# Optimization experiments

Hardware: AMD Instinct MI355X
Metric: run time of the kernel (lower is better)

## Reference

```python
import jax, jax.numpy as jnp
import numpy as np

IMG_C = 256
GC = 32  # graph_channel; must equal graph feature dim 32 for the residual


def setup_inputs() -> dict:
    key = jax.random.key(0)
    ks = jax.random.split(key, 10)
    B, N, WH_SIDE = 8, 4096, 64
    s = lambda fan_in: 1.0 / np.sqrt(fan_in)
    return {
        "input_graph": jax.random.normal(ks[0], (B, N, GC), jnp.float32),
        "input_image": jax.random.normal(ks[1], (B, IMG_C, WH_SIDE, WH_SIDE), jnp.float32),
        # Conv1d(kernel=1) weights stored as [out, in]
        "Wq": jax.random.uniform(ks[2], (GC, 32), jnp.float32, -s(32), s(32)),
        "bq": jax.random.uniform(ks[3], (GC,), jnp.float32, -s(32), s(32)),
        "Wk": jax.random.uniform(ks[4], (GC, IMG_C), jnp.float32, -s(IMG_C), s(IMG_C)),
        "bk": jax.random.uniform(ks[5], (GC,), jnp.float32, -s(IMG_C), s(IMG_C)),
        "Wv": jax.random.uniform(ks[6], (GC, IMG_C), jnp.float32, -s(IMG_C), s(IMG_C)),
        "bv": jax.random.uniform(ks[7], (GC,), jnp.float32, -s(IMG_C), s(IMG_C)),
        "Wc": jax.random.uniform(ks[8], (GC, GC), jnp.float32, -s(GC), s(GC)),
        "bc": jax.random.uniform(ks[9], (GC,), jnp.float32, -s(GC), s(GC)),
    }


def reference(input_graph, input_image, Wq, bq, Wk, bk, Wv, bv, Wc, bc):
    B, C, W, H = input_image.shape
    img = input_image.reshape(B, C, W * H)                      # [B, C, L]
    # 1x1 conv projections == channel matmuls
    K = jnp.einsum('oc,bcl->bol', Wk, img) + bk[None, :, None]  # [B, GC, L]
    V = jnp.einsum('oc,bcl->bol', Wv, img) + bv[None, :, None]  # [B, GC, L]
    # Q: graph [B, N, 32] -> conv over channel dim -> [B, N, GC]
    Q = jnp.einsum('oc,bnc->bno', Wq, input_graph) + bq[None, None, :]
    att = jnp.einsum('bno,bol->bnl', Q, K) / jnp.sqrt(jnp.float32(GC))  # [B, N, L]
    # NOTE: original softmax is over dim=1 (the node/query axis)
    att = jax.nn.softmax(att, axis=1)
    message = jnp.einsum('bol,bnl->bon', V, att)                # [B, GC, N]
    out = input_graph.transpose(0, 2, 1) + (
        jnp.einsum('oc,bcn->bon', Wc, message) + bc[None, :, None]
    )                                                           # [B, GC, N]
    return out.transpose(0, 2, 1)                               # [B, N, GC]
```

## Files before the change

kernel.cpp:

```cpp
#include <hip/hip_runtime.h>

#define BB 8
#define NN 4096
#define LL 4096
#define CC 256

typedef short bf16x8 __attribute__((ext_vector_type(8)));
typedef _Float16 f16x8 __attribute__((ext_vector_type(8)));
typedef __fp16 hf16x2 __attribute__((ext_vector_type(2)));
typedef float f32x4 __attribute__((ext_vector_type(4)));

__device__ __forceinline__ short f2bf(float f) {
  union { float f; unsigned u; } v; v.f = f;
  unsigned r = v.u + 0x7fffu + ((v.u >> 16) & 1u);
  return (short)(r >> 16);
}
__device__ __forceinline__ bf16x8 ld8(const float* __restrict__ fp) {
  float4 a = *(const float4*)fp;
  float4 b = *(const float4*)(fp + 4);
  bf16x8 r;
  r[0] = f2bf(a.x); r[1] = f2bf(a.y); r[2] = f2bf(a.z); r[3] = f2bf(a.w);
  r[4] = f2bf(b.x); r[5] = f2bf(b.y); r[6] = f2bf(b.z); r[7] = f2bf(b.w);
  return r;
}

__global__ __launch_bounds__(256) void ka_proj(
    const float* __restrict__ graph, const float* __restrict__ img,
    const float* __restrict__ Wq, const float* __restrict__ bq,
    const float* __restrict__ Wk, const float* __restrict__ bk,
    const float* __restrict__ Wv, const float* __restrict__ bv,
    short* __restrict__ Qb, short* __restrict__ Kt, _Float16* __restrict__ Vt,
    float* __restrict__ Zbuf)
{
  const int tid = threadIdx.x;
  const int w = tid >> 6, lane = tid & 63, lo = lane & 15, q = lane >> 4;
  const int bid = blockIdx.x;
  if (bid < 512) {
    const int b = bid >> 6;
    if (tid < 64) Zbuf[(size_t)b * LL + ((bid & 63) << 6) + tid] = 0.0f;
    const int lt = ((bid & 63) << 6) + (w << 4);
    f32x4 aK0 = {0,0,0,0}, aK1 = {0,0,0,0}, aV0 = {0,0,0,0}, aV1 = {0,0,0,0};
    const float* ib = img + (size_t)b * CC * LL + lt + lo;
    #pragma unroll
    for (int cs = 0; cs < 8; ++cs) {
      const int c0 = cs * 32 + q * 8;
      bf16x8 bi;
      #pragma unroll
      for (int j = 0; j < 8; ++j) bi[j] = f2bf(ib[(size_t)(c0 + j) * LL]);
      bf16x8 wk0 = ld8(Wk + lo * CC + c0);
      bf16x8 wk1 = ld8(Wk + (lo + 16) * CC + c0);
      bf16x8 wv0 = ld8(Wv + lo * CC + c0);
      bf16x8 wv1 = ld8(Wv + (lo + 16) * CC + c0);
      aK0 = __builtin_amdgcn_mfma_f32_16x16x32_bf16(wk0, bi, aK0, 0, 0, 0);
      aK1 = __builtin_amdgcn_mfma_f32_16x16x32_bf16(wk1, bi, aK1, 0, 0, 0);
      aV0 = __builtin_amdgcn_mfma_f32_16x16x32_bf16(wv0, bi, aV0, 0, 0, 0);
      aV1 = __builtin_amdgcn_mfma_f32_16x16x32_bf16(wv1, bi, aV1, 0, 0, 0);
    }
    const float kscale = 0.2550348663f;
    const size_t row = ((size_t)b * LL + lt + lo) * 32;
    short4 s0, s1;
    s0.x = f2bf((aK0[0] + bk[q * 4 + 0]) * kscale);
    s0.y = f2bf((aK0[1] + bk[q * 4 + 1]) * kscale);
    s0.z = f2bf((aK0[2] + bk[q * 4 + 2]) * kscale);
    s0.w = f2bf((aK0[3] + bk[q * 4 + 3]) * kscale);
    s1.x = f2bf((aK1[0] + bk[16 + q * 4 + 0]) * kscale);
    s1.y = f2bf((aK1[1] + bk[16 + q * 4 + 1]) * kscale);
    s1.z = f2bf((aK1[2] + bk[16 + q * 4 + 2]) * kscale);
    s1.w = f2bf((aK1[3] + bk[16 + q * 4 + 3]) * kscale);
    *(short4*)(Kt + row + q * 4) = s0;
    *(short4*)(Kt + row + 16 + q * 4) = s1;
    union { hf16x2 h[2]; uint2 u; } p0, p1;
    p0.h[0] = __builtin_amdgcn_cvt_pkrtz(aV0[0] + bv[q * 4 + 0], aV0[1] + bv[q * 4 + 1]);
    p0.h[1] = __builtin_amdgcn_cvt_pkrtz(aV0[2] + bv[q * 4 + 2], aV0[3] + bv[q * 4 + 3]);
    p1.h[0] = __builtin_amdgcn_cvt_pkrtz(aV1[0] + bv[16 + q * 4 + 0], aV1[1] + bv[16 + q * 4 + 1]);
    p1.h[1] = __builtin_amdgcn_cvt_pkrtz(aV1[2] + bv[16 + q * 4 + 2], aV1[3] + bv[16 + q * 4 + 3]);
    *(uint2*)(Vt + row + q * 4) = p0.u;
    *(uint2*)(Vt + row + 16 + q * 4) = p1.u;
  } else {
    const int t = bid - 512;
    const int b = t >> 6;
    const int nt = ((t & 63) << 6) + (w << 4);
    bf16x8 ag = ld8(graph + ((size_t)b * NN + nt + lo) * 32 + q * 8);
    bf16x8 w0 = ld8(Wq + lo * 32 + q * 8);
    bf16x8 w1 = ld8(Wq + (lo + 16) * 32 + q * 8);
    f32x4 z = {0,0,0,0};
    f32x4 a0 = __builtin_amdgcn_mfma_f32_16x16x32_bf16(ag, w0, z, 0, 0, 0);
    f32x4 a1 = __builtin_amdgcn_mfma_f32_16x16x32_bf16(ag, w1, z, 0, 0, 0);
    const float b0 = bq[lo], b1 = bq[lo + 16];
    #pragma unroll
    for (int r = 0; r < 4; ++r) {
      const size_t rowq = ((size_t)b * NN + nt + q * 4 + r) * 32;
      Qb[rowq + lo] = f2bf(a0[r] + b0);
      Qb[rowq + 16 + lo] = f2bf(a1[r] + b1);
    }
  }
}

__global__ __launch_bounds__(256) void kb1_z(
    const short* __restrict__ Qb, const short* __restrict__ Kt,
    float* __restrict__ Z)
{
  const int tid = threadIdx.x;
  const int w = tid >> 6, lane = tid & 63, lo = lane & 15, q = lane >> 4;
  const int bid = blockIdx.x;
  const int b = bid & 7;
  const int t = bid >> 3;
  const int l0 = (t & 63) << 6;
  const int nq = t >> 6;
  bf16x8 kf[4];
  #pragma unroll
  for (int f = 0; f < 4; ++f)
    kf[f] = *(const bf16x8*)(Kt + ((size_t)b * LL + l0 + f * 16 + lo) * 32 + q * 8);
  float za[4][4] = {{0}};
  const short* qbase = Qb + ((size_t)b * NN + nq * 1024 + w * 256 + lo) * 32 + q * 8;
  #pragma unroll 4
  for (int it = 0; it < 16; ++it) {
    bf16x8 qf = *(const bf16x8*)(qbase + it * 512);
    #pragma unroll
    for (int f = 0; f < 4; ++f) {
      f32x4 z = {0,0,0,0};
      f32x4 c = __builtin_amdgcn_mfma_f32_16x16x32_bf16(kf[f], qf, z, 0, 0, 0);
      #pragma unroll
      for (int r = 0; r < 4; ++r) za[f][r] += __builtin_amdgcn_exp2f(c[r]);
    }
  }
  #pragma unroll
  for (int m = 1; m < 16; m <<= 1)
    #pragma unroll
    for (int f = 0; f < 4; ++f)
      #pragma unroll
      for (int r = 0; r < 4; ++r)
        za[f][r] += __shfl_xor(za[f][r], m, 64);
  if (lo == 0) {
    #pragma unroll
    for (int f = 0; f < 4; ++f)
      #pragma unroll
      for (int r = 0; r < 4; ++r)
        atomicAdd(&Z[(size_t)b * LL + l0 + f * 16 + q * 4 + r], za[f][r]);
  }
}

__global__ __launch_bounds__(256) void kb2_scale(
    const _Float16* __restrict__ Vt, const float* __restrict__ Z,
    _Float16* __restrict__ Vpp)
{
  const int tid = threadIdx.x;
  const int b = blockIdx.x >> 6;
  const int l = ((blockIdx.x & 63) << 6) + (tid & 63);
  const int og = tid >> 6;
  const float inv = __builtin_amdgcn_rcpf(Z[(size_t)b * LL + l]) * 4096.0f;
  const f16x8 vv = *(const f16x8*)(Vt + ((size_t)b * LL + l) * 32 + og * 8);
  #pragma unroll
  for (int j = 0; j < 8; ++j)
    Vpp[((size_t)b * 32 + og * 8 + j) * LL + l] = (_Float16)((float)vv[j] * inv);
}

#define KC_BODY(LC, PWR, PRD, DOPV)                                           \
  {                                                                           \
    const int lbase_ = (LC) * 64;                                             \
    const int lcn_ = ((LC) + 1 < lc0 + 16) ? (LC) + 1 : (LC);                 \
    bf16x8 kfN_[4];                                                           \
    _Pragma("unroll")                                                         \
    for (int f = 0; f < 4; ++f)                                               \
      kfN_[f] = *(const bf16x8*)(ktb + (size_t)(lcn_ * 64 + f * 16) * 32);    \
    f16x8 vN0_ = *(const f16x8*)(vb0 + lbase_ + q * 8);                       \
    f16x8 vN1_ = *(const f16x8*)(vb0 + lbase_ + 32 + q * 8);                  \
    f16x8 vN2_ = *(const f16x8*)(vb1 + lbase_ + q * 8);                       \
    f16x8 vN3_ = *(const f16x8*)(vb1 + lbase_ + 32 + q * 8);                  \
    _Pragma("unroll")                                                         \
    for (int f = 0; f < 4; ++f) {                                             \
      f32x4 z_ = {0, 0, 0, 0};                                                \
      f32x4 c0_ = __builtin_amdgcn_mfma_f32_16x16x32_bf16(kfC[f], qf0, z_, 0, 0, 0); \
      f32x4 c1_ = __builtin_amdgcn_mfma_f32_16x16x32_bf16(kfC[f], qf1, z_, 0, 0, 0); \
      union { hf16x2 h[2]; uint2 u; } pk0_, pk1_;                             \
      pk0_.h[0] = __builtin_amdgcn_cvt_pkrtz(__builtin_amdgcn_exp2f(c0_[0]),  \
                                             __builtin_amdgcn_exp2f(c0_[1])); \
      pk0_.h[1] = __builtin_amdgcn_cvt_pkrtz(__builtin_amdgcn_exp2f(c0_[2]),  \
                                             __builtin_amdgcn_exp2f(c0_[3])); \
      pk1_.h[0] = __builtin_amdgcn_cvt_pkrtz(__builtin_amdgcn_exp2f(c1_[0]),  \
                                             __builtin_amdgcn_exp2f(c1_[1])); \
      pk1_.h[1] = __builtin_amdgcn_cvt_pkrtz(__builtin_amdgcn_exp2f(c1_[2]),  \
                                             __builtin_amdgcn_exp2f(c1_[3])); \
      *(uint2*)&(PWR)[lo * 72 + f * 16 + q * 4] = pk0_.u;                     \
      *(uint2*)&(PWR)[(16 + lo) * 72 + f * 16 + q * 4] = pk1_.u;              \
    }                                                                         \
    if (DOPV) {                                                               \
      f16x8 pa00_ = *(const f16x8*)&(PRD)[lo * 72 + q * 8];                   \
      f16x8 pa01_ = *(const f16x8*)&(PRD)[lo * 72 + 32 + q * 8];              \
      f16x8 pa10_ = *(const f16x8*)&(PRD)[(16 + lo) * 72 + q * 8];            \
      f16x8 pa11_ = *(const f16x8*)&(PRD)[(16 + lo) * 72 + 32 + q * 8];       \
      m00 = __builtin_amdgcn_mfma_f32_16x16x32_f16(pa00_, vC0, m00, 0, 0, 0); \
      m10 = __builtin_amdgcn_mfma_f32_16x16x32_f16(pa10_, vC0, m10, 0, 0, 0); \
      m01 = __builtin_amdgcn_mfma_f32_16x16x32_f16(pa00_, vC2, m01, 0, 0, 0); \
      m11 = __builtin_amdgcn_mfma_f32_16x16x32_f16(pa10_, vC2, m11, 0, 0, 0); \
      m00 = __builtin_amdgcn_mfma_f32_16x16x32_f16(pa01_, vC1, m00, 0, 0, 0); \
      m10 = __builtin_amdgcn_mfma_f32_16x16x32_f16(pa11_, vC1, m10, 0, 0, 0); \
      m01 = __builtin_amdgcn_mfma_f32_16x16x32_f16(pa01_, vC3, m01, 0, 0, 0); \
      m11 = __builtin_amdgcn_mfma_f32_16x16x32_f16(pa11_, vC3, m11, 0, 0, 0); \
    }                                                                         \
    vC0 = vN0_; vC1 = vN1_; vC2 = vN2_; vC3 = vN3_;                           \
    _Pragma("unroll")                                                         \
    for (int f = 0; f < 4; ++f) kfC[f] = kfN_[f];                             \
  }

__global__ __launch_bounds__(256, 4) void kc_attn(
    const short* __restrict__ Qb, const short* __restrict__ Kt,
    const _Float16* __restrict__ Vpp, const float* __restrict__ graph,
    const float* __restrict__ Wc, const float* __restrict__ bc,
    float* __restrict__ out)
{
  __shared__ __align__(16) unsigned char smem[4 * 2 * 32 * 72 * 2];
  const int tid = threadIdx.x;
  const int w = tid >> 6, lane = tid & 63, lo = lane & 15, q = lane >> 4;
  const int b = blockIdx.x & 7;
  const int n0 = (blockIdx.x >> 3) << 5;
  _Float16* PA = (_Float16*)smem + (w * 2 + 0) * (32 * 72);
  _Float16* PB = (_Float16*)smem + (w * 2 + 1) * (32 * 72);
  float* MS = (float*)smem;
  const bf16x8 qf0 = *(const bf16x8*)(Qb + ((size_t)b * NN + n0 + lo) * 32 + q * 8);
  const bf16x8 qf1 = *(const bf16x8*)(Qb + ((size_t)b * NN + n0 + 16 + lo) * 32 + q * 8);
  f32x4 m00 = {0,0,0,0}, m01 = {0,0,0,0}, m10 = {0,0,0,0}, m11 = {0,0,0,0};
  const short* ktb = Kt + (size_t)b * LL * 32 + lo * 32 + q * 8;
  const _Float16* vb0 = Vpp + ((size_t)b * 32 + lo) * LL;
  const _Float16* vb1 = vb0 + (size_t)16 * LL;
  const int lc0 = w * 16;
  bf16x8 kfC[4];
  #pragma unroll
  for (int f = 0; f < 4; ++f)
    kfC[f] = *(const bf16x8*)(ktb + (size_t)(lc0 * 64 + f * 16) * 32);
  f16x8 vC0 = {0,0,0,0,0,0,0,0}, vC1 = {0,0,0,0,0,0,0,0};
  f16x8 vC2 = {0,0,0,0,0,0,0,0}, vC3 = {0,0,0,0,0,0,0,0};
  #pragma unroll 1
  for (int i2 = 0; i2 < 8; ++i2) {
    const int lce = lc0 + i2 * 2;
    KC_BODY(lce, PA, PB, (i2 != 0));
    KC_BODY(lce + 1, PB, PA, true);
  }
  {
    f16x8 pa00_ = *(const f16x8*)&PB[lo * 72 + q * 8];
    f16x8 pa01_ = *(const f16x8*)&PB[lo * 72 + 32 + q * 8];
    f16x8 pa10_ = *(const f16x8*)&PB[(16 + lo) * 72 + q * 8];
    f16x8 pa11_ = *(const f16x8*)&PB[(16 + lo) * 72 + 32 + q * 8];
    m00 = __builtin_amdgcn_mfma_f32_16x16x32_f16(pa00_, vC0, m00, 0, 0, 0);
    m10 = __builtin_amdgcn_mfma_f32_16x16x32_f16(pa10_, vC0, m10, 0, 0, 0);
    m01 = __builtin_amdgcn_mfma_f32_16x16x32_f16(pa00_, vC2, m01, 0, 0, 0);
    m11 = __builtin_amdgcn_mfma_f32_16x16x32_f16(pa10_, vC2, m11, 0, 0, 0);
    m00 = __builtin_amdgcn_mfma_f32_16x16x32_f16(pa01_, vC1, m00, 0, 0, 0);
    m10 = __builtin_amdgcn_mfma_f32_16x16x32_f16(pa11_, vC1, m10, 0, 0, 0);
    m01 = __builtin_amdgcn_mfma_f32_16x16x32_f16(pa01_, vC3, m01, 0, 0, 0);
    m11 = __builtin_amdgcn_mfma_f32_16x16x32_f16(pa11_, vC3, m11, 0, 0, 0);
  }
  float* MSw = MS + w * 2304;
  #pragma unroll
  for (int r = 0; r < 4; ++r) {
    MSw[(q * 4 + r) * 36 + lo] = m00[r];
    MSw[(q * 4 + r) * 36 + 16 + lo] = m01[r];
    MSw[(16 + q * 4 + r) * 36 + lo] = m10[r];
    MSw[(16 + q * 4 + r) * 36 + 16 + lo] = m11[r];
  }
  __syncthreads();
  const int o = lane & 31, nh = lane >> 5;
  float wcr[32];
  #pragma unroll
  for (int c4 = 0; c4 < 8; ++c4) {
    float4 wc4 = *(const float4*)(Wc + o * 32 + c4 * 4);
    wcr[c4 * 4 + 0] = wc4.x * (1.0f / 4096.0f);
    wcr[c4 * 4 + 1] = wc4.y * (1.0f / 4096.0f);
    wcr[c4 * 4 + 2] = wc4.z * (1.0f / 4096.0f);
    wcr[c4 * 4 + 3] = wc4.w * (1.0f / 4096.0f);
  }
  const float bcv = bc[o];
  #pragma unroll
  for (int rr = 0; rr < 4; ++rr) {
    const int nl = w * 8 + nh * 4 + rr;
    f32x4 s = {0,0,0,0};
    #pragma unroll
    for (int cc = 0; cc < 8; ++cc) {
      f32x4 ma = *(const f32x4*)&MS[0 * 2304 + nl * 36 + cc * 4];
      f32x4 mb = *(const f32x4*)&MS[1 * 2304 + nl * 36 + cc * 4];
      f32x4 mc = *(const f32x4*)&MS[2 * 2304 + nl * 36 + cc * 4];
      f32x4 md = *(const f32x4*)&MS[3 * 2304 + nl * 36 + cc * 4];
      f32x4 m4 = ma + mb + mc + md;
      s[0] += wcr[cc * 4 + 0] * m4[0];
      s[1] += wcr[cc * 4 + 1] * m4[1];
      s[2] += wcr[cc * 4 + 2] * m4[2];
      s[3] += wcr[cc * 4 + 3] * m4[3];
    }
    const size_t idx = ((size_t)b * NN + n0 + nl) * 32 + o;
    out[idx] = s[0] + s[1] + s[2] + s[3] + bcv + graph[idx];
  }
}

extern "C" void kernel_launch(void* const* d_in, const int* in_sizes, int n_in,
                              void* d_out, int out_size, void* d_ws, size_t ws_size,
                              hipStream_t stream) {
  const float* graph = (const float*)d_in[0];
  const float* img   = (const float*)d_in[1];
  const float* Wq    = (const float*)d_in[2];
  const float* bq    = (const float*)d_in[3];
  const float* Wk    = (const float*)d_in[4];
  const float* bk    = (const float*)d_in[5];
  const float* Wv    = (const float*)d_in[6];
  const float* bv    = (const float*)d_in[7];
  const float* Wc    = (const float*)d_in[8];
  const float* bc    = (const float*)d_in[9];
  char* ws = (char*)d_ws;
  short*    Qb  = (short*)(ws + 0);
  short*    Kt  = (short*)(ws + 2097152);
  _Float16* Vt  = (_Float16*)(ws + 4194304);
  _Float16* Vpp = (_Float16*)(ws + 6291456);
  float*    Zb  = (float*)(ws + 8388608);
  ka_proj<<<dim3(1024), dim3(256), 0, stream>>>(graph, img, Wq, bq, Wk, bk, Wv, bv,
                                                Qb, Kt, Vt, Zb);
  kb1_z<<<dim3(2048), dim3(256), 0, stream>>>(Qb, Kt, Zb);
  kb2_scale<<<dim3(512), dim3(256), 0, stream>>>(Vt, Zb, Vpp);
  kc_attn<<<dim3(1024), dim3(256), 0, stream>>>(Qb, Kt, Vpp, graph, Wc, bc,
                                                (float*)d_out);
}
```

Before: 185.3 us.

## Fuse all stages into one cooperative kernel with grid syncs, fold normalization into attention

Merges the four launches into a single cooperative kernel whose phases are separated by grid-wide syncs, with a four-kernel fallback if the cooperative launch fails. The projection now writes V directly in channel-major layout, and the separate V-rescale pass is replaced by a small reciprocal-Z table. The attention phase multiplies each exp by that reciprocal before packing. The Z phase is rebalanced to 1024 blocks with twice the loop length. This removes launch gaps and one full pass over V, at the cost of grid-sync overhead, an extra multiply per element in the hot loop, and strided scalar V stores.

```diff
diff --git a/kernel.cpp b/kernel.cpp
--- a/kernel.cpp
+++ b/kernel.cpp
@@ -1,4 +1,5 @@
 #include <hip/hip_runtime.h>
+#include <hip/hip_cooperative_groups.h>
 
 #define BB 8
 #define NN 4096
@@ -24,20 +25,18 @@
   return r;
 }
 
-__global__ __launch_bounds__(256) void ka_proj(
+__device__ __forceinline__ void phase0(
+    int bid, int tid, int w, int lo, int q,
     const float* __restrict__ graph, const float* __restrict__ img,
     const float* __restrict__ Wq, const float* __restrict__ bq,
     const float* __restrict__ Wk, const float* __restrict__ bk,
     const float* __restrict__ Wv, const float* __restrict__ bv,
-    short* __restrict__ Qb, short* __restrict__ Kt, _Float16* __restrict__ Vt,
-    float* __restrict__ Zbuf)
-{
-  const int tid = threadIdx.x;
-  const int w = tid >> 6, lane = tid & 63, lo = lane & 15, q = lane >> 4;
-  const int bid = blockIdx.x;
+    short* __restrict__ Qb, short* __restrict__ Kt,
+    _Float16* __restrict__ Vt2, float* __restrict__ Zb)
+{
   if (bid < 512) {
     const int b = bid >> 6;
-    if (tid < 64) Zbuf[(size_t)b * LL + ((bid & 63) << 6) + tid] = 0.0f;
+    if (tid < 64) Zb[(size_t)b * LL + ((bid & 63) << 6) + tid] = 0.0f;
     const int lt = ((bid & 63) << 6) + (w << 4);
     f32x4 aK0 = {0,0,0,0}, aK1 = {0,0,0,0}, aV0 = {0,0,0,0}, aV1 = {0,0,0,0};
     const float* ib = img + (size_t)b * CC * LL + lt + lo;
@@ -69,13 +68,17 @@
     s1.w = f2bf((aK1[3] + bk[16 + q * 4 + 3]) * kscale);
     *(short4*)(Kt + row + q * 4) = s0;
     *(short4*)(Kt + row + 16 + q * 4) = s1;
-    union { hf16x2 h[2]; uint2 u; } p0, p1;
+    union { hf16x2 h[2]; __fp16 e[4]; } p0, p1;
     p0.h[0] = __builtin_amdgcn_cvt_pkrtz(aV0[0] + bv[q * 4 + 0], aV0[1] + bv[q * 4 + 1]);
     p0.h[1] = __builtin_amdgcn_cvt_pkrtz(aV0[2] + bv[q * 4 + 2], aV0[3] + bv[q * 4 + 3]);
     p1.h[0] = __builtin_amdgcn_cvt_pkrtz(aV1[0] + bv[16 + q * 4 + 0], aV1[1] + bv[16 + q * 4 + 1]);
     p1.h[1] = __builtin_amdgcn_cvt_pkrtz(aV1[2] + bv[16 + q * 4 + 2], aV1[3] + bv[16 + q * 4 + 3]);
-    *(uint2*)(Vt + row + q * 4) = p0.u;
-    *(uint2*)(Vt + row + 16 + q * 4) = p1.u;
+    const size_t vbase = (size_t)b * 32 * LL + lt + lo;
+    #pragma unroll
+    for (int r = 0; r < 4; ++r) {
+      Vt2[vbase + (size_t)(q * 4 + r) * LL] = p0.e[r];
+      Vt2[vbase + (size_t)(16 + q * 4 + r) * LL] = p1.e[r];
+    }
   } else {
     const int t = bid - 512;
     const int b = t >> 6;
@@ -96,25 +99,23 @@
   }
 }
 
-__global__ __launch_bounds__(256) void kb1_z(
+__device__ __forceinline__ void phase1(
+    int bid, int w, int lo, int q,
     const short* __restrict__ Qb, const short* __restrict__ Kt,
-    float* __restrict__ Z)
-{
-  const int tid = threadIdx.x;
-  const int w = tid >> 6, lane = tid & 63, lo = lane & 15, q = lane >> 4;
-  const int bid = blockIdx.x;
+    float* __restrict__ Zb)
+{
   const int b = bid & 7;
   const int t = bid >> 3;
-  const int l0 = (t & 63) << 6;
-  const int nq = t >> 6;
+  const int l0 = (t >> 1) << 6;
+  const int nbase = (t & 1) * 2048 + w * 512;
   bf16x8 kf[4];
   #pragma unroll
   for (int f = 0; f < 4; ++f)
     kf[f] = *(const bf16x8*)(Kt + ((size_t)b * LL + l0 + f * 16 + lo) * 32 + q * 8);
   float za[4][4] = {{0}};
-  const short* qbase = Qb + ((size_t)b * NN + nq * 1024 + w * 256 + lo) * 32 + q * 8;
+  const short* qbase = Qb + ((size_t)b * NN + nbase + lo) * 32 + q * 8;
   #pragma unroll 4
-  for (int it = 0; it < 16; ++it) {
+  for (int it = 0; it < 32; ++it) {
     bf16x8 qf = *(const bf16x8*)(qbase + it * 512);
     #pragma unroll
     for (int f = 0; f < 4; ++f) {
@@ -136,29 +137,27 @@
     for (int f = 0; f < 4; ++f)
       #pragma unroll
       for (int r = 0; r < 4; ++r)
-        atomicAdd(&Z[(size_t)b * LL + l0 + f * 16 + q * 4 + r], za[f][r]);
-  }
-}
-
-__global__ __launch_bounds__(256) void kb2_scale(
-    const _Float16* __restrict__ Vt, const float* __restrict__ Z,
-    _Float16* __restrict__ Vpp)
-{
-  const int tid = threadIdx.x;
-  const int b = blockIdx.x >> 6;
-  const int l = ((blockIdx.x & 63) << 6) + (tid & 63);
-  const int og = tid >> 6;
-  const float inv = __builtin_amdgcn_rcpf(Z[(size_t)b * LL + l]) * 4096.0f;
-  const f16x8 vv = *(const f16x8*)(Vt + ((size_t)b * LL + l) * 32 + og * 8);
-  #pragma unroll
-  for (int j = 0; j < 8; ++j)
-    Vpp[((size_t)b * 32 + og * 8 + j) * LL + l] = (_Float16)((float)vv[j] * inv);
+        atomicAdd(&Zb[(size_t)b * LL + l0 + f * 16 + q * 4 + r], za[f][r]);
+  }
+}
+
+__device__ __forceinline__ void phase2(
+    int bid, int tid, const float* __restrict__ Zb, float* __restrict__ Zi)
+{
+  if (tid < 32) {
+    const int i = bid * 32 + tid;
+    Zi[i] = 4096.0f * __builtin_amdgcn_rcpf(Zb[i]);
+  }
 }
 
 #define KC_BODY(LC, PWR, PRD, DOPV)                                           \
   {                                                                           \
     const int lbase_ = (LC) * 64;                                             \
     const int lcn_ = ((LC) + 1 < lc0 + 16) ? (LC) + 1 : (LC);                 \
+    float4 zi_[4];                                                            \
+    _Pragma("unroll")                                                         \
+    for (int f = 0; f < 4; ++f)                                               \
+      zi_[f] = *(const float4*)(zib + lbase_ + f * 16);                       \
     bf16x8 kfN_[4];                                                           \
     _Pragma("unroll")                                                         \
     for (int f = 0; f < 4; ++f)                                               \
@@ -173,14 +172,18 @@
       f32x4 c0_ = __builtin_amdgcn_mfma_f32_16x16x32_bf16(kfC[f], qf0, z_, 0, 0, 0); \
       f32x4 c1_ = __builtin_amdgcn_mfma_f32_16x16x32_bf16(kfC[f], qf1, z_, 0, 0, 0); \
       union { hf16x2 h[2]; uint2 u; } pk0_, pk1_;                             \
-      pk0_.h[0] = __builtin_amdgcn_cvt_pkrtz(__builtin_amdgcn_exp2f(c0_[0]),  \
-                                             __builtin_amdgcn_exp2f(c0_[1])); \
-      pk0_.h[1] = __builtin_amdgcn_cvt_pkrtz(__builtin_amdgcn_exp2f(c0_[2]),  \
-                                             __builtin_amdgcn_exp2f(c0_[3])); \
-      pk1_.h[0] = __builtin_amdgcn_cvt_pkrtz(__builtin_amdgcn_exp2f(c1_[0]),  \
-                                             __builtin_amdgcn_exp2f(c1_[1])); \
-      pk1_.h[1] = __builtin_amdgcn_cvt_pkrtz(__builtin_amdgcn_exp2f(c1_[2]),  \
-                                             __builtin_amdgcn_exp2f(c1_[3])); \
+      pk0_.h[0] = __builtin_amdgcn_cvt_pkrtz(                                 \
+          __builtin_amdgcn_exp2f(c0_[0]) * zi_[f].x,                          \
+          __builtin_amdgcn_exp2f(c0_[1]) * zi_[f].y);                         \
+      pk0_.h[1] = __builtin_amdgcn_cvt_pkrtz(                                 \
+          __builtin_amdgcn_exp2f(c0_[2]) * zi_[f].z,                          \
+          __builtin_amdgcn_exp2f(c0_[3]) * zi_[f].w);                         \
+      pk1_.h[0] = __builtin_amdgcn_cvt_pkrtz(                                 \
+          __builtin_amdgcn_exp2f(c1_[0]) * zi_[f].x,                          \
+          __builtin_amdgcn_exp2f(c1_[1]) * zi_[f].y);                         \
+      pk1_.h[1] = __builtin_amdgcn_cvt_pkrtz(                                 \
+          __builtin_amdgcn_exp2f(c1_[2]) * zi_[f].z,                          \
+          __builtin_amdgcn_exp2f(c1_[3]) * zi_[f].w);                         \
       *(uint2*)&(PWR)[lo * 72 + f * 16 + q * 4] = pk0_.u;                     \
       *(uint2*)&(PWR)[(16 + lo) * 72 + f * 16 + q * 4] = pk1_.u;              \
     }                                                                         \
@@ -203,17 +206,17 @@
     for (int f = 0; f < 4; ++f) kfC[f] = kfN_[f];                             \
   }
 
-__global__ __launch_bounds__(256, 4) void kc_attn(
+__device__ __forceinline__ void phase3(
+    int bid, int tid, int w, int lo, int q,
     const short* __restrict__ Qb, const short* __restrict__ Kt,
-    const _Float16* __restrict__ Vpp, const float* __restrict__ graph,
-    const float* __restrict__ Wc, const float* __restrict__ bc,
-    float* __restrict__ out)
+    const _Float16* __restrict__ Vt2, const float* __restrict__ Zi,
+    const float* __restrict__ graph, const float* __restrict__ Wc,
+    const float* __restrict__ bc, float* __restrict__ out)
 {
   __shared__ __align__(16) unsigned char smem[4 * 2 * 32 * 72 * 2];
-  const int tid = threadIdx.x;
-  const int w = tid >> 6, lane = tid & 63, lo = lane & 15, q = lane >> 4;
-  const int b = blockIdx.x & 7;
-  const int n0 = (blockIdx.x >> 3) << 5;
+  const int lane = tid & 63;
+  const int b = bid & 7;
+  const int n0 = (bid >> 3) << 5;
   _Float16* PA = (_Float16*)smem + (w * 2 + 0) * (32 * 72);
   _Float16* PB = (_Float16*)smem + (w * 2 + 1) * (32 * 72);
   float* MS = (float*)smem;
@@ -221,8 +224,9 @@
   const bf16x8 qf1 = *(const bf16x8*)(Qb + ((size_t)b * NN + n0 + 16 + lo) * 32 + q * 8);
   f32x4 m00 = {0,0,0,0}, m01 = {0,0,0,0}, m10 = {0,0,0,0}, m11 = {0,0,0,0};
   const short* ktb = Kt + (size_t)b * LL * 32 + lo * 32 + q * 8;
-  const _Float16* vb0 = Vpp + ((size_t)b * 32 + lo) * LL;
+  const _Float16* vb0 = Vt2 + ((size_t)b * 32 + lo) * LL;
   const _Float16* vb1 = vb0 + (size_t)16 * LL;
+  const float* zib = Zi + b * 4096 + q * 4;
   const int lc0 = w * 16;
   bf16x8 kfC[4];
   #pragma unroll
@@ -289,6 +293,63 @@
     const size_t idx = ((size_t)b * NN + n0 + nl) * 32 + o;
     out[idx] = s[0] + s[1] + s[2] + s[3] + bcv + graph[idx];
   }
+}
+
+__global__ __launch_bounds__(256, 4) void fused_all(
+    const float* __restrict__ graph, const float* __restrict__ img,
+    const float* __restrict__ Wq, const float* __restrict__ bq,
+    const float* __restrict__ Wk, const float* __restrict__ bk,
+    const float* __restrict__ Wv, const float* __restrict__ bv,
+    const float* __restrict__ Wc, const float* __restrict__ bc,
+    short* __restrict__ Qb, short* __restrict__ Kt, _Float16* __restrict__ Vt2,
+    float* __restrict__ Zb, float* __restrict__ Zi, float* __restrict__ out)
+{
+  cooperative_groups::grid_group grid = cooperative_groups::this_grid();
+  const int tid = threadIdx.x;
+  const int w = tid >> 6, lane = tid & 63, lo = lane & 15, q = lane >> 4;
+  const int bid = blockIdx.x;
+  phase0(bid, tid, w, lo, q, graph, img, Wq, bq, Wk, bk, Wv, bv, Qb, Kt, Vt2, Zb);
+  grid.sync();
+  phase1(bid, w, lo, q, Qb, Kt, Zb);
+  grid.sync();
+  phase2(bid, tid, Zb, Zi);
+  grid.sync();
+  phase3(bid, tid, w, lo, q, Qb, Kt, Vt2, Zi, graph, Wc, bc, out);
+}
+
+__global__ __launch_bounds__(256, 4) void k_p0(
+    const float* __restrict__ graph, const float* __restrict__ img,
+    const float* __restrict__ Wq, const float* __restrict__ bq,
+    const float* __restrict__ Wk, const float* __restrict__ bk,
+    const float* __restrict__ Wv, const float* __restrict__ bv,
+    short* __restrict__ Qb, short* __restrict__ Kt, _Float16* __restrict__ Vt2,
+    float* __restrict__ Zb)
+{
+  const int tid = threadIdx.x;
+  phase0(blockIdx.x, tid, tid >> 6, tid & 15, (tid & 63) >> 4,
+         graph, img, Wq, bq, Wk, bk, Wv, bv, Qb, Kt, Vt2, Zb);
+}
+__global__ __launch_bounds__(256, 4) void k_p1(
+    const short* __restrict__ Qb, const short* __restrict__ Kt,
+    float* __restrict__ Zb)
+{
+  const int tid = threadIdx.x;
+  phase1(blockIdx.x, tid >> 6, tid & 15, (tid & 63) >> 4, Qb, Kt, Zb);
+}
+__global__ __launch_bounds__(256, 4) void k_p2(
+    const float* __restrict__ Zb, float* __restrict__ Zi)
+{
+  phase2(blockIdx.x, threadIdx.x, Zb, Zi);
+}
+__global__ __launch_bounds__(256, 4) void k_p3(
+    const short* __restrict__ Qb, const short* __restrict__ Kt,
+    const _Float16* __restrict__ Vt2, const float* __restrict__ Zi,
+    const float* __restrict__ graph, const float* __restrict__ Wc,
+    const float* __restrict__ bc, float* __restrict__ out)
+{
+  const int tid = threadIdx.x;
+  phase3(blockIdx.x, tid, tid >> 6, tid & 15, (tid & 63) >> 4,
+         Qb, Kt, Vt2, Zi, graph, Wc, bc, out);
 }
 
 extern "C" void kernel_launch(void* const* d_in, const int* in_sizes, int n_in,
@@ -307,13 +368,21 @@
   char* ws = (char*)d_ws;
   short*    Qb  = (short*)(ws + 0);
   short*    Kt  = (short*)(ws + 2097152);
-  _Float16* Vt  = (_Float16*)(ws + 4194304);
-  _Float16* Vpp = (_Float16*)(ws + 6291456);
-  float*    Zb  = (float*)(ws + 8388608);
-  ka_proj<<<dim3(1024), dim3(256), 0, stream>>>(graph, img, Wq, bq, Wk, bk, Wv, bv,
-                                                Qb, Kt, Vt, Zb);
-  kb1_z<<<dim3(2048), dim3(256), 0, stream>>>(Qb, Kt, Zb);
-  kb2_scale<<<dim3(512), dim3(256), 0, stream>>>(Vt, Zb, Vpp);
-  kc_attn<<<dim3(1024), dim3(256), 0, stream>>>(Qb, Kt, Vpp, graph, Wc, bc,
-                                                (float*)d_out);
-}
+  _Float16* Vt2 = (_Float16*)(ws + 4194304);
+  float*    Zb  = (float*)(ws + 6291456);
+  float*    Zi  = (float*)(ws + 6422528);
+  float*    outp = (float*)d_out;
+  void* args[] = {
+    (void*)&graph, (void*)&img, (void*)&Wq, (void*)&bq, (void*)&Wk, (void*)&bk,
+    (void*)&Wv, (void*)&bv, (void*)&Wc, (void*)&bc,
+    (void*)&Qb, (void*)&Kt, (void*)&Vt2, (void*)&Zb, (void*)&Zi, (void*)&outp};
+  hipError_t err = hipLaunchCooperativeKernel((const void*)fused_all,
+                                              dim3(1024), dim3(256), args, 0, stream);
+  if (err != hipSuccess) {
+    k_p0<<<dim3(1024), dim3(256), 0, stream>>>(graph, img, Wq, bq, Wk, bk, Wv, bv,
+                                               Qb, Kt, Vt2, Zb);
+    k_p1<<<dim3(1024), dim3(256), 0, stream>>>(Qb, Kt, Zb);
+    k_p2<<<dim3(1024), dim3(256), 0, stream>>>(Zb, Zi);
+    k_p3<<<dim3(1024), dim3(256), 0, stream>>>(Qb, Kt, Vt2, Zi, graph, Wc, bc, outp);
+  }
+}
```

Measured after the change: 541.8 us. +192.4%, slower.
